# Optimization experiments

Hardware: AMD Instinct MI355X
Metric: run time of the kernel (lower is better)

The kernel has to match this reference:

```python
import jax, jax.numpy as jnp
import numpy as np

N = 100000      # nodes
E = 1200000     # edges
D_IN = 128      # input_dim
H = 64          # hidden_dim
OUT = 3         # output_dim
EPS = 1e-5      # BatchNorm eps


def setup_inputs() -> dict:
    key = jax.random.key(0)
    ks = jax.random.split(key, 24)
    w = lambda k, shape: jax.random.normal(k, shape, jnp.float32) * 0.05
    return {
        "x": jax.random.normal(ks[0], (N, D_IN), jnp.float32),
        "edge_index": jax.random.randint(ks[1], (2, E), 0, N, dtype=jnp.int32),
        "proj_W": w(ks[2], (H, D_IN)), "proj_b": w(ks[3], (H,)),
        "conv1_W": w(ks[4], (H, H)), "conv1_b": w(ks[5], (H,)),
        "bn1_g": jnp.ones((H,), jnp.float32), "bn1_b": w(ks[6], (H,)),
        "conv2_W": w(ks[7], (H, H)), "conv2_b": w(ks[8], (H,)),
        "bn2_g": jnp.ones((H,), jnp.float32), "bn2_b": w(ks[9], (H,)),
        "conv3_W": w(ks[10], (H, H)), "conv3_b": w(ks[11], (H,)),
        "bn3_g": jnp.ones((H,), jnp.float32), "bn3_b": w(ks[12], (H,)),
        "byp_W": w(ks[13], (OUT, D_IN)), "byp_b": w(ks[14], (OUT,)),
        "head_W": w(ks[15], (OUT, H + OUT)), "head_b": w(ks[16], (OUT,)),
    }


def reference(x, edge_index, proj_W, proj_b,
              conv1_W, conv1_b, bn1_g, bn1_b,
              conv2_W, conv2_b, bn2_g, bn2_b,
              conv3_W, conv3_b, bn3_g, bn3_b,
              byp_W, byp_b, head_W, head_b):
    n = x.shape[0]
    row, col = edge_index[0], edge_index[1]
    loop = jnp.arange(n, dtype=row.dtype)
    row_f = jnp.concatenate([row, loop])   # source (with self loops)
    col_f = jnp.concatenate([col, loop])   # target
    # symmetric GCN normalization: deg over targets of A+I, edge weight 1
    deg = jax.ops.segment_sum(jnp.ones(row_f.shape, jnp.float32), col_f, num_segments=n)
    dinv = jnp.where(deg > 0, jax.lax.rsqrt(deg), 0.0)
    norm = dinv[row_f] * dinv[col_f]       # [E+N]

    def gcn(h, W, b):
        h = h @ W.T                                    # transform then propagate
        msg = h[row_f] * norm[:, None]                 # gather + scale
        return jax.ops.segment_sum(msg, col_f, num_segments=n) + b

    def bn(h, g, b):
        # eval-mode BatchNorm1d: running_mean=0, running_var=1 buffers
        return h * (g / jnp.sqrt(1.0 + EPS)) + b

    h = x @ proj_W.T + proj_b
    idn = h
    h = jax.nn.relu(bn(gcn(h, conv1_W, conv1_b), bn1_g, bn1_b)) + idn  # dropout inactive (eval)
    idn = h
    h = jax.nn.relu(bn(gcn(h, conv2_W, conv2_b), bn2_g, bn2_b)) + idn
    h = jax.nn.relu(bn(gcn(h, conv3_W, conv3_b), bn3_g, bn3_b))

    byp = x @ byp_W.T + byp_b
    p = jnp.concatenate([h, byp], axis=1) @ head_W.T + head_b
    kappa = jnp.clip(p[:, 0] * 5.0 + 2.5, 0.2, 10.0)
    alpha = p[:, 1]
    tau = jnp.clip(p[:, 2] + 0.5, 0.05, 2.0)
    return jnp.stack([kappa, alpha, tau], axis=1)
```

## Files before the change

### kernel.cpp

```cpp
#include <hip/hip_runtime.h>
#include <hip/hip_fp16.h>

#define NN 100000
#define NE 1200000
#define NBUK ((NN + 127) / 128)
#define NCHUNK 512

typedef _Float16 h8 __attribute__((ext_vector_type(8)));
typedef float f32x4 __attribute__((ext_vector_type(4)));
typedef float f32x2 __attribute__((ext_vector_type(2)));

__global__ __launch_bounds__(256) void k_bucketA(const int* __restrict__ col,
                                                 int* __restrict__ blkcnt) {
    __shared__ int lh[NBUK];
    const int tid = threadIdx.x;
    const int per = (NE + NCHUNK - 1) / NCHUNK;
    const int e0 = blockIdx.x * per;
    const int e1 = (e0 + per < NE) ? (e0 + per) : NE;
    for (int i = tid; i < NBUK; i += 256) lh[i] = 0;
    __syncthreads();
    for (int e = e0 + tid; e < e1; e += 256)
        atomicAdd(&lh[col[e] >> 7], 1);
    __syncthreads();
    for (int b = tid; b < NBUK; b += 256)
        blkcnt[b * NCHUNK + blockIdx.x] = lh[b];
}

__global__ __launch_bounds__(512) void k_colscan(int* __restrict__ blkcnt, int* __restrict__ bcnt) {
    __shared__ int s[NCHUNK];
    const int b = blockIdx.x, tid = threadIdx.x;
    int v = blkcnt[b * NCHUNK + tid];
    s[tid] = v;
    __syncthreads();
    #pragma unroll
    for (int d = 1; d < NCHUNK; d <<= 1) {
        int t = (tid >= d) ? s[tid - d] : 0;
        __syncthreads();
        s[tid] += t;
        __syncthreads();
    }
    blkcnt[b * NCHUNK + tid] = s[tid] - v;
    if (tid == NCHUNK - 1) bcnt[b] = s[NCHUNK - 1];
}

__global__ __launch_bounds__(1024) void k_bscan(int* __restrict__ bcnt) {
    __shared__ int s[1024];
    int tid = threadIdx.x;
    int v = (tid < NBUK) ? bcnt[tid] : 0;
    s[tid] = v;
    __syncthreads();
    #pragma unroll
    for (int d = 1; d < 1024; d <<= 1) {
        int t = (tid >= d) ? s[tid - d] : 0;
        __syncthreads();
        s[tid] += t;
        __syncthreads();
    }
    if (tid < NBUK) bcnt[tid] = s[tid] - v;
    if (tid == 0) bcnt[NBUK] = NE;
}

__global__ __launch_bounds__(256) void k_bucketB(const int* __restrict__ row,
                                                 const int* __restrict__ col,
                                                 const int* __restrict__ bbase,
                                                 const int* __restrict__ blkcnt,
                                                 unsigned* __restrict__ tmp) {
    __shared__ int lh[NBUK];
    const int tid = threadIdx.x;
    const int per = (NE + NCHUNK - 1) / NCHUNK;
    const int e0 = blockIdx.x * per;
    const int e1 = (e0 + per < NE) ? (e0 + per) : NE;
    for (int b = tid; b < NBUK; b += 256)
        lh[b] = bbase[b] + blkcnt[b * NCHUNK + blockIdx.x];
    __syncthreads();
    for (int e = e0 + tid; e < e1; e += 256) {
        int c = col[e], r = row[e];
        int pos = atomicAdd(&lh[c >> 7], 1);
        tmp[pos] = ((unsigned)r << 7) | (unsigned)(c & 127);
    }
}

__global__ __launch_bounds__(256) void k_build(const unsigned* __restrict__ tmp,
                                               const int* __restrict__ bbase,
                                               int* __restrict__ off,
                                               float* __restrict__ dinv,
                                               int* __restrict__ csr_row) {
    __shared__ int cnt[128], s[128], cur[128];
    const int b = blockIdx.x, tid = threadIdx.x;
    const int colBase = b << 7;
    const int nCols = (NN - colBase < 128) ? (NN - colBase) : 128;
    const int seg0 = bbase[b], seg1 = bbase[b + 1];
    if (tid < 128) cnt[tid] = 0;
    __syncthreads();
    for (int i = seg0 + tid; i < seg1; i += 256)
        atomicAdd(&cnt[tmp[i] & 127], 1);
    __syncthreads();
    if (tid < 128) s[tid] = cnt[tid];
    __syncthreads();
    #pragma unroll
    for (int d = 1; d < 128; d <<= 1) {
        int t = (tid < 128 && tid >= d) ? s[tid - d] : 0;
        __syncthreads();
        if (tid < 128) s[tid] += t;
        __syncthreads();
    }
    if (tid < nCols) {
        int exc = seg0 + s[tid] - cnt[tid];
        off[colBase + tid] = exc;
        cur[tid] = exc;
        dinv[colBase + tid] = rsqrtf((float)cnt[tid] + 1.0f);
    }
    if (b == 0 && tid == 0) off[NN] = NE;
    __syncthreads();
    for (int i = seg0 + tid; i < seg1; i += 256) {
        unsigned v = tmp[i];
        int pos = atomicAdd(&cur[v & 127u], 1);
        csr_row[pos] = (int)(v >> 7);
    }
}

__global__ __launch_bounds__(256) void k_gemmPC(const float* __restrict__ X,
                                                const float* __restrict__ W,
                                                const float* __restrict__ bias,
                                                _Float16* __restrict__ Yh,
                                                const float* __restrict__ bypW,
                                                const float* __restrict__ bypb,
                                                float* __restrict__ bypOut,
                                                const float* __restrict__ convW1,
                                                const float* __restrict__ dinv,
                                                unsigned char* __restrict__ Y8,
                                                int n_nodes) {
    constexpr int D = 128, RS = D + 8, KS = D / 32;
    constexpr int RS2 = 72;
    __shared__ _Float16 Xh[64 * RS];
    __shared__ _Float16 Wh[64 * RS];
    const int tid = threadIdx.x;
    const int n0 = blockIdx.x * 64;

    for (int i = tid; i < 64 * (D / 8); i += 256) {
        int j = i / (D / 8), d8 = (i % (D / 8)) * 8;
        const float4* wp = (const float4*)&W[j * D + d8];
        float4 w0 = wp[0], w1 = wp[1];
        h8 h = { (_Float16)w0.x, (_Float16)w0.y, (_Float16)w0.z, (_Float16)w0.w,
                 (_Float16)w1.x, (_Float16)w1.y, (_Float16)w1.z, (_Float16)w1.w };
        *(h8*)&Wh[j * RS + d8] = h;
    }
    for (int i = tid; i < 64 * (D / 8); i += 256) {
        int nl = i / (D / 8), d8 = (i % (D / 8)) * 8;
        int n = n0 + nl; if (n >= n_nodes) n = n_nodes - 1;
        const float4* xp = (const float4*)&X[(size_t)n * D + d8];
        float4 x0 = xp[0], x1 = xp[1];
        h8 h = { (_Float16)x0.x, (_Float16)x0.y, (_Float16)x0.z, (_Float16)x0.w,
                 (_Float16)x1.x, (_Float16)x1.y, (_Float16)x1.z, (_Float16)x1.w };
        *(h8*)&Xh[nl * RS + d8] = h;
    }
    __syncthreads();

    const int wid = tid >> 6, lane = tid & 63;
    const int lm = lane & 15, lq = lane >> 4;
    const int mBase = wid * 16;

    h8 bfrag[4][KS];
    #pragma unroll
    for (int t = 0; t < 4; ++t)
        #pragma unroll
        for (int s = 0; s < KS; ++s)
            bfrag[t][s] = *(const h8*)&Wh[(t * 16 + lm) * RS + s * 32 + lq * 8];

    h8 bfragB[KS];
    #pragma unroll
    for (int s = 0; s < KS; ++s) {
        if (lm < 3) {
            const float4* wp = (const float4*)&bypW[lm * D + s * 32 + lq * 8];
            float4 w0 = wp[0], w1 = wp[1];
            bfragB[s] = (h8){ (_Float16)w0.x, (_Float16)w0.y, (_Float16)w0.z, (_Float16)w0.w,
                              (_Float16)w1.x, (_Float16)w1.y, (_Float16)w1.z, (_Float16)w1.w };
        } else {
            bfragB[s] = (h8)(_Float16)0;
        }
    }

    f32x4 acc[5] = {};
    #pragma unroll
    for (int s = 0; s < KS; ++s) {
        h8 a = *(const h8*)&Xh[(mBase + lm) * RS + s * 32 + lq * 8];
        #pragma unroll
        for (int t = 0; t < 4; ++t)
            acc[t] = __builtin_amdgcn_mfma_f32_16x16x32_f16(a, bfrag[t][s], acc[t], 0, 0, 0);
        acc[4] = __builtin_amdgcn_mfma_f32_16x16x32_f16(a, bfragB[s], acc[4], 0, 0, 0);
    }

    float bb[4];
    #pragma unroll
    for (int t = 0; t < 4; ++t) bb[t] = bias[t * 16 + lm];
    float bypbv = (lm < 3) ? bypb[lm] : 0.f;
    const int nodeBase = n0 + mBase + lq * 4;

    __syncthreads();

    #pragma unroll
    for (int r = 0; r < 4; ++r) {
        int node = nodeBase + r;
        int nloc = mBase + lq * 4 + r;
        #pragma unroll
        for (int t = 0; t < 4; ++t) {
            _Float16 hv = (_Float16)(acc[t][r] + bb[t]);
            Xh[nloc * RS2 + t * 16 + lm] = hv;
            if (node < n_nodes)
                Yh[(size_t)node * 64 + t * 16 + lm] = hv;
        }
        if (node < n_nodes && lm < 3)
            bypOut[node * 3 + lm] = acc[4][r] + bypbv;
    }
    for (int i = tid; i < 64 * 8; i += 256) {
        int j = i >> 3, d8 = (i & 7) * 8;
        const float4* wp = (const float4*)&convW1[j * 64 + d8];
        float4 w0 = wp[0], w1 = wp[1];
        h8 h = { (_Float16)w0.x, (_Float16)w0.y, (_Float16)w0.z, (_Float16)w0.w,
                 (_Float16)w1.x, (_Float16)w1.y, (_Float16)w1.z, (_Float16)w1.w };
        *(h8*)&Wh[j * RS2 + d8] = h;
    }
    __syncthreads();

    h8 cfrag[4][2];
    #pragma unroll
    for (int t = 0; t < 4; ++t)
        #pragma unroll
        for (int s = 0; s < 2; ++s)
            cfrag[t][s] = *(const h8*)&Wh[(t * 16 + lm) * RS2 + s * 32 + lq * 8];

    f32x4 acc2[4] = {};
    #pragma unroll
    for (int s = 0; s < 2; ++s) {
        h8 a = *(const h8*)&Xh[(mBase + lm) * RS2 + s * 32 + lq * 8];
        #pragma unroll
        for (int t = 0; t < 4; ++t)
            acc2[t] = __builtin_amdgcn_mfma_f32_16x16x32_f16(a, cfrag[t][s], acc2[t], 0, 0, 0);
    }
    #pragma unroll
    for (int r = 0; r < 4; ++r) {
        int node = nodeBase + r;
        if (node < n_nodes) {
            float sdv = dinv[node];
            #pragma unroll
            for (int t = 0; t < 4; ++t) {
                float v = acc2[t][r] * sdv;
                int pk = __builtin_amdgcn_cvt_pk_fp8_f32(v, v, 0, false);
                Y8[(size_t)node * 64 + t * 16 + lm] = (unsigned char)(pk & 0xff);
            }
        }
    }
}

__global__ __launch_bounds__(256) void k_gemmC(const _Float16* __restrict__ Xhg,
                                               const float* __restrict__ W,
                                               const float* __restrict__ dinv,
                                               unsigned char* __restrict__ Y8,
                                               int n_nodes) {
    constexpr int D = 64, RS = D + 8, KS = D / 32;
    __shared__ _Float16 Xh[64 * RS];
    __shared__ _Float16 Wh[64 * RS];
    const int tid = threadIdx.x;
    const int n0 = blockIdx.x * 64;

    for (int i = tid; i < 64 * (D / 8); i += 256) {
        int j = i / (D / 8), d8 = (i % (D / 8)) * 8;
        const float4* wp = (const float4*)&W[j * D + d8];
        float4 w0 = wp[0], w1 = wp[1];
        h8 h = { (_Float16)w0.x, (_Float16)w0.y, (_Float16)w0.z, (_Float16)w0.w,
                 (_Float16)w1.x, (_Float16)w1.y, (_Float16)w1.z, (_Float16)w1.w };
        *(h8*)&Wh[j * RS + d8] = h;
    }
    for (int i = tid; i < 64 * (D / 8); i += 256) {
        int nl = i / (D / 8), d8 = (i % (D / 8)) * 8;
        int n = n0 + nl; if (n >= n_nodes) n = n_nodes - 1;
        *(h8*)&Xh[nl * RS + d8] = *(const h8*)&Xhg[(size_t)n * D + d8];
    }
    __syncthreads();

    const int wid = tid >> 6, lane = tid & 63;
    const int lm = lane & 15, lq = lane >> 4;
    const int mBase = wid * 16;

    h8 bfrag[4][KS];
    #pragma unroll
    for (int t = 0; t < 4; ++t)
        #pragma unroll
        for (int s = 0; s < KS; ++s)
            bfrag[t][s] = *(const h8*)&Wh[(t * 16 + lm) * RS + s * 32 + lq * 8];

    f32x4 acc[4] = {};
    #pragma unroll
    for (int s = 0; s < KS; ++s) {
        h8 a = *(const h8*)&Xh[(mBase + lm) * RS + s * 32 + lq * 8];
        #pragma unroll
        for (int t = 0; t < 4; ++t)
            acc[t] = __builtin_amdgcn_mfma_f32_16x16x32_f16(a, bfrag[t][s], acc[t], 0, 0, 0);
    }

    const int nodeBase = n0 + mBase + lq * 4;
    #pragma unroll
    for (int r = 0; r < 4; ++r) {
        int node = nodeBase + r;
        if (node < n_nodes) {
            float sdv = dinv[node];
            #pragma unroll
            for (int t = 0; t < 4; ++t) {
                float v = acc[t][r] * sdv;
                int pk = __builtin_amdgcn_cvt_pk_fp8_f32(v, v, 0, false);
                Y8[(size_t)node * 64 + t * 16 + lm] = (unsigned char)(pk & 0xff);
            }
        }
    }
}

template<bool RES, bool HEAD>
__global__ __launch_bounds__(256) void k_gather(const unsigned char* __restrict__ hB8,
                                                const float* __restrict__ dinv,
                                                const int* __restrict__ off,
                                                const int* __restrict__ csr_row,
                                                const float* __restrict__ convb,
                                                const float* __restrict__ bng,
                                                const float* __restrict__ bnb,
                                                _Float16* __restrict__ hA,
                                                const float* __restrict__ byp,
                                                const float* __restrict__ headW,
                                                const float* __restrict__ headb,
                                                float* __restrict__ out) {
    __shared__ float HWs[HEAD ? 204 : 1];
    const int tid = threadIdx.x;
    if constexpr (HEAD) {
        for (int i = tid; i < 204; i += 256)
            HWs[i] = (i < 201) ? headW[i] : headb[i - 201];
        __syncthreads();
    }
    const int wid = tid >> 6, lane = tid & 63;
    const int n = blockIdx.x * 32 + wid * 8 + (lane >> 3);
    const int oct = lane & 7;
    const int f0 = oct * 8;

    const int e0 = off[n], eEnd = off[n + 1];
    const int deg = eEnd - e0;
    int m = deg;
    #pragma unroll
    for (int mask = 8; mask < 64; mask <<= 1) {
        int o = __shfl_xor(m, mask, 64);
        m = (o > m) ? o : m;
    }

    const uint2* rows8 = (const uint2*)hB8;
    float acc[8] = {0, 0, 0, 0, 0, 0, 0, 0};
    uint2 selfw = rows8[(size_t)n * 8 + oct];
    {
        f32x2 p0 = __builtin_amdgcn_cvt_pk_f32_fp8(selfw.x, false);
        f32x2 p1 = __builtin_amdgcn_cvt_pk_f32_fp8(selfw.x, true);
        f32x2 p2 = __builtin_amdgcn_cvt_pk_f32_fp8(selfw.y, false);
        f32x2 p3 = __builtin_amdgcn_cvt_pk_f32_fp8(selfw.y, true);
        acc[0] += p0.x; acc[1] += p0.y; acc[2] += p1.x; acc[3] += p1.y;
        acc[4] += p2.x; acc[5] += p2.y; acc[6] += p3.x; acc[7] += p3.y;
    }
    for (int it = 0; it < m; it += 8) {
        uint2 w[8];
        #pragma unroll
        for (int q = 0; q < 8; ++q) {
            bool vq = it + q < deg;
            int rq = csr_row[vq ? e0 + it + q : 0];
            w[q] = rows8[(size_t)rq * 8 + oct];
            if (!vq) { w[q].x = 0; w[q].y = 0; }
        }
        #pragma unroll
        for (int q = 0; q < 8; ++q) {
            f32x2 p0 = __builtin_amdgcn_cvt_pk_f32_fp8(w[q].x, false);
            f32x2 p1 = __builtin_amdgcn_cvt_pk_f32_fp8(w[q].x, true);
            f32x2 p2 = __builtin_amdgcn_cvt_pk_f32_fp8(w[q].y, false);
            f32x2 p3 = __builtin_amdgcn_cvt_pk_f32_fp8(w[q].y, true);
            acc[0] += p0.x; acc[1] += p0.y; acc[2] += p1.x; acc[3] += p1.y;
            acc[4] += p2.x; acc[5] += p2.y; acc[6] += p3.x; acc[7] += p3.y;
        }
    }

    const float dv = dinv[n];
    const float bnscale = rsqrtf(1.0f + 1e-5f);
    const float4 cb0 = *(const float4*)&convb[f0], cb1 = *(const float4*)&convb[f0 + 4];
    const float4 g0  = *(const float4*)&bng[f0],  g1  = *(const float4*)&bng[f0 + 4];
    const float4 b0_ = *(const float4*)&bnb[f0],  b1_ = *(const float4*)&bnb[f0 + 4];
    const float cb[8] = { cb0.x, cb0.y, cb0.z, cb0.w, cb1.x, cb1.y, cb1.z, cb1.w };
    const float gg[8] = { g0.x, g0.y, g0.z, g0.w, g1.x, g1.y, g1.z, g1.w };
    const float bb[8] = { b0_.x, b0_.y, b0_.z, b0_.w, b1_.x, b1_.y, b1_.z, b1_.w };
    float v[8];
    #pragma unroll
    for (int j = 0; j < 8; ++j)
        v[j] = fmaxf((acc[j] * dv + cb[j]) * (gg[j] * bnscale) + bb[j], 0.0f);

    if constexpr (!HEAD) {
        size_t o = ((size_t)n << 6) + f0;
        if constexpr (RES) {
            h8 old = *(const h8*)&hA[o];
            #pragma unroll
            for (int j = 0; j < 8; ++j) v[j] += (float)old[j];
        }
        h8 res = { (_Float16)v[0], (_Float16)v[1], (_Float16)v[2], (_Float16)v[3],
                   (_Float16)v[4], (_Float16)v[5], (_Float16)v[6], (_Float16)v[7] };
        *(h8*)&hA[o] = res;
    } else {
        float p[3];
        #pragma unroll
        for (int o = 0; o < 3; ++o) {
            float t = 0.f;
            #pragma unroll
            for (int j = 0; j < 8; ++j) t += v[j] * HWs[o * 67 + f0 + j];
            p[o] = t;
        }
        #pragma unroll
        for (int mask = 1; mask < 8; mask <<= 1) {
            #pragma unroll
            for (int o = 0; o < 3; ++o) p[o] += __shfl_xor(p[o], mask, 64);
        }
        if (oct == 0) {
            float by0 = byp[n * 3], by1 = byp[n * 3 + 1], by2 = byp[n * 3 + 2];
            #pragma unroll
            for (int o = 0; o < 3; ++o)
                p[o] += by0 * HWs[o * 67 + 64] + by1 * HWs[o * 67 + 65] + by2 * HWs[o * 67 + 66]
                      + HWs[201 + o];
            float kappa = fminf(fmaxf(p[0] * 5.0f + 2.5f, 0.2f), 10.0f);
            float tau   = fminf(fmaxf(p[2] + 0.5f, 0.05f), 2.0f);
            out[(size_t)n * 3]     = kappa;
            out[(size_t)n * 3 + 1] = p[1];
            out[(size_t)n * 3 + 2] = tau;
        }
    }
}

extern "C" void kernel_launch(void* const* d_in, const int* in_sizes, int n_in,
                              void* d_out, int out_size, void* d_ws, size_t ws_size,
                              hipStream_t stream) {
    const float* x     = (const float*)d_in[0];
    const int*   ei    = (const int*)d_in[1];
    const int*   row   = ei;
    const int*   col   = ei + NE;
    const float* projW = (const float*)d_in[2];
    const float* projb = (const float*)d_in[3];
    const float* convW[3] = { (const float*)d_in[4], (const float*)d_in[8],  (const float*)d_in[12] };
    const float* convb[3] = { (const float*)d_in[5], (const float*)d_in[9],  (const float*)d_in[13] };
    const float* bng[3]   = { (const float*)d_in[6], (const float*)d_in[10], (const float*)d_in[14] };
    const float* bnb[3]   = { (const float*)d_in[7], (const float*)d_in[11], (const float*)d_in[15] };
    const float* bypW  = (const float*)d_in[16];
    const float* bypb  = (const float*)d_in[17];
    const float* headW = (const float*)d_in[18];
    const float* headb = (const float*)d_in[19];
    float* out = (float*)d_out;

    float*    ws   = (float*)d_ws;
    float*    dinv = ws;
    _Float16* hAh  = (_Float16*)(ws + 102400);
    unsigned char* hB8 = (unsigned char*)(hAh + (size_t)NN * 64);
    float*    byp  = (float*)(hB8 + (size_t)NN * 64);
    int*      off     = (int*)(byp + 300032);
    int*      csr_row = off + 100096;
    int*      bcnt    = csr_row + NE;
    int*      blkcnt  = bcnt + 784;
    unsigned* tmp     = (unsigned*)hAh;

    k_bucketA<<<NCHUNK, 256, 0, stream>>>(col, blkcnt);
    k_colscan<<<NBUK, NCHUNK, 0, stream>>>(blkcnt, bcnt);
    k_bscan<<<1, 1024, 0, stream>>>(bcnt);
    k_bucketB<<<NCHUNK, 256, 0, stream>>>(row, col, bcnt, blkcnt, tmp);
    k_build<<<NBUK, 256, 0, stream>>>(tmp, bcnt, off, dinv, csr_row);

    k_gemmPC<<<(NN + 63) / 64, 256, 0, stream>>>(
        x, projW, projb, hAh, bypW, bypb, byp, convW[0], dinv, hB8, NN);

    for (int l = 0; l < 3; l++) {
        if (l > 0)
            k_gemmC<<<(NN + 63) / 64, 256, 0, stream>>>(hAh, convW[l], dinv, hB8, NN);
        if (l < 2)
            k_gather<true, false><<<NN / 32, 256, 0, stream>>>(
                hB8, dinv, off, csr_row, convb[l], bng[l], bnb[l], hAh,
                nullptr, nullptr, nullptr, nullptr);
        else
            k_gather<false, true><<<NN / 32, 256, 0, stream>>>(
                hB8, dinv, off, csr_row, convb[l], bng[l], bnb[l], nullptr,
                byp, headW, headb, out);
    }
}
```

Baseline: 256.8 us.

## Fuse next-layer GEMM into gather epilogue and merge scan kernels

The separate per-layer transform GEMM kernel is removed and its work moved into the gather kernel's epilogue. Each block stages its 32 freshly aggregated fp16 rows in shared memory and multiplies them by the next layer's weights with MFMA, writing fp8 output into a ping-pong buffer. The bucket-count scans are merged into one launch, with bucket totals accumulated atomically after a memset, and the gather loop now iterates per node degree rather than the max degree across the wave. This removes two kernel launches and one round trip of the hidden state through memory per layer. In exchange the gather kernel uses more shared memory and a block barrier, and needs an extra fp8 buffer.

```diff
diff --git a/kernel.cpp b/kernel.cpp
--- a/kernel.cpp
+++ b/kernel.cpp
@@ -11,7 +11,8 @@
 typedef float f32x2 __attribute__((ext_vector_type(2)));
 
 __global__ __launch_bounds__(256) void k_bucketA(const int* __restrict__ col,
-                                                 int* __restrict__ blkcnt) {
+                                                 int* __restrict__ blkcnt,
+                                                 int* __restrict__ bcnt) {
     __shared__ int lh[NBUK];
     const int tid = threadIdx.x;
     const int per = (NE + NCHUNK - 1) / NCHUNK;
@@ -22,42 +23,43 @@
     for (int e = e0 + tid; e < e1; e += 256)
         atomicAdd(&lh[col[e] >> 7], 1);
     __syncthreads();
-    for (int b = tid; b < NBUK; b += 256)
-        blkcnt[b * NCHUNK + blockIdx.x] = lh[b];
-}
-
-__global__ __launch_bounds__(512) void k_colscan(int* __restrict__ blkcnt, int* __restrict__ bcnt) {
-    __shared__ int s[NCHUNK];
+    for (int b = tid; b < NBUK; b += 256) {
+        int v = lh[b];
+        blkcnt[b * NCHUNK + blockIdx.x] = v;
+        if (v) atomicAdd(&bcnt[b], v);
+    }
+}
+
+__global__ __launch_bounds__(1024) void k_scanAll(int* __restrict__ blkcnt,
+                                                  int* __restrict__ bcnt) {
+    __shared__ int s[1024];
     const int b = blockIdx.x, tid = threadIdx.x;
-    int v = blkcnt[b * NCHUNK + tid];
-    s[tid] = v;
-    __syncthreads();
-    #pragma unroll
-    for (int d = 1; d < NCHUNK; d <<= 1) {
-        int t = (tid >= d) ? s[tid - d] : 0;
-        __syncthreads();
-        s[tid] += t;
-        __syncthreads();
-    }
-    blkcnt[b * NCHUNK + tid] = s[tid] - v;
-    if (tid == NCHUNK - 1) bcnt[b] = s[NCHUNK - 1];
-}
-
-__global__ __launch_bounds__(1024) void k_bscan(int* __restrict__ bcnt) {
-    __shared__ int s[1024];
-    int tid = threadIdx.x;
-    int v = (tid < NBUK) ? bcnt[tid] : 0;
-    s[tid] = v;
-    __syncthreads();
-    #pragma unroll
-    for (int d = 1; d < 1024; d <<= 1) {
-        int t = (tid >= d) ? s[tid - d] : 0;
-        __syncthreads();
-        s[tid] += t;
-        __syncthreads();
-    }
-    if (tid < NBUK) bcnt[tid] = s[tid] - v;
-    if (tid == 0) bcnt[NBUK] = NE;
+    if (b < NBUK) {
+        int v = (tid < NCHUNK) ? blkcnt[b * NCHUNK + tid] : 0;
+        s[tid] = v;
+        __syncthreads();
+        #pragma unroll
+        for (int d = 1; d < 1024; d <<= 1) {
+            int t = (tid >= d) ? s[tid - d] : 0;
+            __syncthreads();
+            s[tid] += t;
+            __syncthreads();
+        }
+        if (tid < NCHUNK) blkcnt[b * NCHUNK + tid] = s[tid] - v;
+    } else {
+        int v = (tid < NBUK) ? bcnt[tid] : 0;
+        s[tid] = v;
+        __syncthreads();
+        #pragma unroll
+        for (int d = 1; d < 1024; d <<= 1) {
+            int t = (tid >= d) ? s[tid - d] : 0;
+            __syncthreads();
+            s[tid] += t;
+            __syncthreads();
+        }
+        if (tid < NBUK) bcnt[tid] = s[tid] - v;
+        if (tid == 0) bcnt[NBUK] = NE;
+    }
 }
 
 __global__ __launch_bounds__(256) void k_bucketB(const int* __restrict__ row,
@@ -252,69 +254,16 @@
     }
 }
 
-__global__ __launch_bounds__(256) void k_gemmC(const _Float16* __restrict__ Xhg,
-                                               const float* __restrict__ W,
-                                               const float* __restrict__ dinv,
-                                               unsigned char* __restrict__ Y8,
-                                               int n_nodes) {
-    constexpr int D = 64, RS = D + 8, KS = D / 32;
-    __shared__ _Float16 Xh[64 * RS];
-    __shared__ _Float16 Wh[64 * RS];
-    const int tid = threadIdx.x;
-    const int n0 = blockIdx.x * 64;
-
-    for (int i = tid; i < 64 * (D / 8); i += 256) {
-        int j = i / (D / 8), d8 = (i % (D / 8)) * 8;
-        const float4* wp = (const float4*)&W[j * D + d8];
-        float4 w0 = wp[0], w1 = wp[1];
-        h8 h = { (_Float16)w0.x, (_Float16)w0.y, (_Float16)w0.z, (_Float16)w0.w,
-                 (_Float16)w1.x, (_Float16)w1.y, (_Float16)w1.z, (_Float16)w1.w };
-        *(h8*)&Wh[j * RS + d8] = h;
-    }
-    for (int i = tid; i < 64 * (D / 8); i += 256) {
-        int nl = i / (D / 8), d8 = (i % (D / 8)) * 8;
-        int n = n0 + nl; if (n >= n_nodes) n = n_nodes - 1;
-        *(h8*)&Xh[nl * RS + d8] = *(const h8*)&Xhg[(size_t)n * D + d8];
-    }
-    __syncthreads();
-
-    const int wid = tid >> 6, lane = tid & 63;
-    const int lm = lane & 15, lq = lane >> 4;
-    const int mBase = wid * 16;
-
-    h8 bfrag[4][KS];
-    #pragma unroll
-    for (int t = 0; t < 4; ++t)
-        #pragma unroll
-        for (int s = 0; s < KS; ++s)
-            bfrag[t][s] = *(const h8*)&Wh[(t * 16 + lm) * RS + s * 32 + lq * 8];
-
-    f32x4 acc[4] = {};
-    #pragma unroll
-    for (int s = 0; s < KS; ++s) {
-        h8 a = *(const h8*)&Xh[(mBase + lm) * RS + s * 32 + lq * 8];
-        #pragma unroll
-        for (int t = 0; t < 4; ++t)
-            acc[t] = __builtin_amdgcn_mfma_f32_16x16x32_f16(a, bfrag[t][s], acc[t], 0, 0, 0);
-    }
-
-    const int nodeBase = n0 + mBase + lq * 4;
-    #pragma unroll
-    for (int r = 0; r < 4; ++r) {
-        int node = nodeBase + r;
-        if (node < n_nodes) {
-            float sdv = dinv[node];
-            #pragma unroll
-            for (int t = 0; t < 4; ++t) {
-                float v = acc[t][r] * sdv;
-                int pk = __builtin_amdgcn_cvt_pk_fp8_f32(v, v, 0, false);
-                Y8[(size_t)node * 64 + t * 16 + lm] = (unsigned char)(pk & 0xff);
-            }
-        }
-    }
-}
-
-template<bool RES, bool HEAD>
+__device__ __forceinline__ void acc_fp8(float* acc, uint2 w) {
+    f32x2 p0 = __builtin_amdgcn_cvt_pk_f32_fp8(w.x, false);
+    f32x2 p1 = __builtin_amdgcn_cvt_pk_f32_fp8(w.x, true);
+    f32x2 p2 = __builtin_amdgcn_cvt_pk_f32_fp8(w.y, false);
+    f32x2 p3 = __builtin_amdgcn_cvt_pk_f32_fp8(w.y, true);
+    acc[0] += p0.x; acc[1] += p0.y; acc[2] += p1.x; acc[3] += p1.y;
+    acc[4] += p2.x; acc[5] += p2.y; acc[6] += p3.x; acc[7] += p3.y;
+}
+
+template<bool HEAD>
 __global__ __launch_bounds__(256) void k_gather(const unsigned char* __restrict__ hB8,
                                                 const float* __restrict__ dinv,
                                                 const int* __restrict__ off,
@@ -323,60 +272,56 @@
                                                 const float* __restrict__ bng,
                                                 const float* __restrict__ bnb,
                                                 _Float16* __restrict__ hA,
+                                                const float* __restrict__ nextW,
+                                                unsigned char* __restrict__ Y8,
                                                 const float* __restrict__ byp,
                                                 const float* __restrict__ headW,
                                                 const float* __restrict__ headb,
                                                 float* __restrict__ out) {
+    constexpr int RS2 = 72;
+    __shared__ _Float16 Ws[HEAD ? 1 : 64 * RS2];
+    __shared__ _Float16 Hs[HEAD ? 1 : 32 * RS2];
     __shared__ float HWs[HEAD ? 204 : 1];
     const int tid = threadIdx.x;
     if constexpr (HEAD) {
         for (int i = tid; i < 204; i += 256)
             HWs[i] = (i < 201) ? headW[i] : headb[i - 201];
         __syncthreads();
+    } else {
+        for (int i = tid; i < 64 * 8; i += 256) {
+            int j = i >> 3, d8 = (i & 7) * 8;
+            const float4* wp = (const float4*)&nextW[j * 64 + d8];
+            float4 w0 = wp[0], w1 = wp[1];
+            h8 h = { (_Float16)w0.x, (_Float16)w0.y, (_Float16)w0.z, (_Float16)w0.w,
+                     (_Float16)w1.x, (_Float16)w1.y, (_Float16)w1.z, (_Float16)w1.w };
+            *(h8*)&Ws[j * RS2 + d8] = h;
+        }
     }
     const int wid = tid >> 6, lane = tid & 63;
-    const int n = blockIdx.x * 32 + wid * 8 + (lane >> 3);
+    const int nloc = wid * 8 + (lane >> 3);
+    const int n = blockIdx.x * 32 + nloc;
     const int oct = lane & 7;
     const int f0 = oct * 8;
 
-    const int e0 = off[n], eEnd = off[n + 1];
-    const int deg = eEnd - e0;
-    int m = deg;
-    #pragma unroll
-    for (int mask = 8; mask < 64; mask <<= 1) {
-        int o = __shfl_xor(m, mask, 64);
-        m = (o > m) ? o : m;
-    }
+    const int e0 = off[n];
+    const int deg = off[n + 1] - e0;
 
     const uint2* rows8 = (const uint2*)hB8;
     float acc[8] = {0, 0, 0, 0, 0, 0, 0, 0};
-    uint2 selfw = rows8[(size_t)n * 8 + oct];
-    {
-        f32x2 p0 = __builtin_amdgcn_cvt_pk_f32_fp8(selfw.x, false);
-        f32x2 p1 = __builtin_amdgcn_cvt_pk_f32_fp8(selfw.x, true);
-        f32x2 p2 = __builtin_amdgcn_cvt_pk_f32_fp8(selfw.y, false);
-        f32x2 p3 = __builtin_amdgcn_cvt_pk_f32_fp8(selfw.y, true);
-        acc[0] += p0.x; acc[1] += p0.y; acc[2] += p1.x; acc[3] += p1.y;
-        acc[4] += p2.x; acc[5] += p2.y; acc[6] += p3.x; acc[7] += p3.y;
-    }
-    for (int it = 0; it < m; it += 8) {
+    acc_fp8(acc, rows8[(size_t)n * 8 + oct]);
+
+    for (int it = 0; it < deg; it += 8) {
+        const int rem = deg - it;
         uint2 w[8];
         #pragma unroll
         for (int q = 0; q < 8; ++q) {
-            bool vq = it + q < deg;
-            int rq = csr_row[vq ? e0 + it + q : 0];
+            int rq = csr_row[e0 + it + ((q < rem) ? q : 0)];
             w[q] = rows8[(size_t)rq * 8 + oct];
-            if (!vq) { w[q].x = 0; w[q].y = 0; }
-        }
-        #pragma unroll
-        for (int q = 0; q < 8; ++q) {
-            f32x2 p0 = __builtin_amdgcn_cvt_pk_f32_fp8(w[q].x, false);
-            f32x2 p1 = __builtin_amdgcn_cvt_pk_f32_fp8(w[q].x, true);
-            f32x2 p2 = __builtin_amdgcn_cvt_pk_f32_fp8(w[q].y, false);
-            f32x2 p3 = __builtin_amdgcn_cvt_pk_f32_fp8(w[q].y, true);
-            acc[0] += p0.x; acc[1] += p0.y; acc[2] += p1.x; acc[3] += p1.y;
-            acc[4] += p2.x; acc[5] += p2.y; acc[6] += p3.x; acc[7] += p3.y;
-        }
+            if (q >= rem) { w[q].x = 0; w[q].y = 0; }
+        }
+        #pragma unroll
+        for (int q = 0; q < 8; ++q)
+            acc_fp8(acc, w[q]);
     }
 
     const float dv = dinv[n];
@@ -394,14 +339,45 @@
 
     if constexpr (!HEAD) {
         size_t o = ((size_t)n << 6) + f0;
-        if constexpr (RES) {
-            h8 old = *(const h8*)&hA[o];
-            #pragma unroll
-            for (int j = 0; j < 8; ++j) v[j] += (float)old[j];
-        }
+        h8 old = *(const h8*)&hA[o];
+        #pragma unroll
+        for (int j = 0; j < 8; ++j) v[j] += (float)old[j];
         h8 res = { (_Float16)v[0], (_Float16)v[1], (_Float16)v[2], (_Float16)v[3],
                    (_Float16)v[4], (_Float16)v[5], (_Float16)v[6], (_Float16)v[7] };
         *(h8*)&hA[o] = res;
+        *(h8*)&Hs[nloc * RS2 + f0] = res;
+        __syncthreads();
+
+        const int lm = lane & 15, lq = lane >> 4;
+        const int mt = (wid & 1) * 16;
+        const int nt = (wid >> 1) * 32;
+        h8 afrag[2], bfrag[2][2];
+        #pragma unroll
+        for (int s = 0; s < 2; ++s)
+            afrag[s] = *(const h8*)&Hs[(mt + lm) * RS2 + s * 32 + lq * 8];
+        #pragma unroll
+        for (int t = 0; t < 2; ++t)
+            #pragma unroll
+            for (int s = 0; s < 2; ++s)
+                bfrag[t][s] = *(const h8*)&Ws[(nt + t * 16 + lm) * RS2 + s * 32 + lq * 8];
+        f32x4 acc2[2] = {};
+        #pragma unroll
+        for (int s = 0; s < 2; ++s)
+            #pragma unroll
+            for (int t = 0; t < 2; ++t)
+                acc2[t] = __builtin_amdgcn_mfma_f32_16x16x32_f16(afrag[s], bfrag[t][s], acc2[t], 0, 0, 0);
+        const int nodeBase = blockIdx.x * 32 + mt + lq * 4;
+        #pragma unroll
+        for (int r = 0; r < 4; ++r) {
+            int node = nodeBase + r;
+            float sdv = dinv[node];
+            #pragma unroll
+            for (int t = 0; t < 2; ++t) {
+                float vv = acc2[t][r] * sdv;
+                int pk = __builtin_amdgcn_cvt_pk_fp8_f32(vv, vv, 0, false);
+                Y8[(size_t)node * 64 + nt + t * 16 + lm] = (unsigned char)(pk & 0xff);
+            }
+        }
     } else {
         float p[3];
         #pragma unroll
@@ -453,33 +429,31 @@
     float*    ws   = (float*)d_ws;
     float*    dinv = ws;
     _Float16* hAh  = (_Float16*)(ws + 102400);
-    unsigned char* hB8 = (unsigned char*)(hAh + (size_t)NN * 64);
-    float*    byp  = (float*)(hB8 + (size_t)NN * 64);
+    unsigned char* hB8a = (unsigned char*)(hAh + (size_t)NN * 64);
+    float*    byp  = (float*)(hB8a + (size_t)NN * 64);
     int*      off     = (int*)(byp + 300032);
     int*      csr_row = off + 100096;
     int*      bcnt    = csr_row + NE;
     int*      blkcnt  = bcnt + 784;
+    unsigned char* hB8b = (unsigned char*)(blkcnt + (size_t)NBUK * NCHUNK);
     unsigned* tmp     = (unsigned*)hAh;
 
-    k_bucketA<<<NCHUNK, 256, 0, stream>>>(col, blkcnt);
-    k_colscan<<<NBUK, NCHUNK, 0, stream>>>(blkcnt, bcnt);
-    k_bscan<<<1, 1024, 0, stream>>>(bcnt);
+    hipMemsetAsync(bcnt, 0, 784 * sizeof(int), stream);
+    k_bucketA<<<NCHUNK, 256, 0, stream>>>(col, blkcnt, bcnt);
+    k_scanAll<<<NBUK + 1, 1024, 0, stream>>>(blkcnt, bcnt);
     k_bucketB<<<NCHUNK, 256, 0, stream>>>(row, col, bcnt, blkcnt, tmp);
     k_build<<<NBUK, 256, 0, stream>>>(tmp, bcnt, off, dinv, csr_row);
 
     k_gemmPC<<<(NN + 63) / 64, 256, 0, stream>>>(
-        x, projW, projb, hAh, bypW, bypb, byp, convW[0], dinv, hB8, NN);
-
-    for (int l = 0; l < 3; l++) {
-        if (l > 0)
-            k_gemmC<<<(NN + 63) / 64, 256, 0, stream>>>(hAh, convW[l], dinv, hB8, NN);
-        if (l < 2)
-            k_gather<true, false><<<NN / 32, 256, 0, stream>>>(
-                hB8, dinv, off, csr_row, convb[l], bng[l], bnb[l], hAh,
-                nullptr, nullptr, nullptr, nullptr);
-        else
-            k_gather<false, true><<<NN / 32, 256, 0, stream>>>(
-                hB8, dinv, off, csr_row, convb[l], bng[l], bnb[l], nullptr,
-                byp, headW, headb, out);
-    }
-}
+        x, projW, projb, hAh, bypW, bypb, byp, convW[0], dinv, hB8a, NN);
+
+    k_gather<false><<<NN / 32, 256, 0, stream>>>(
+        hB8a, dinv, off, csr_row, convb[0], bng[0], bnb[0], hAh,
+        convW[1], hB8b, nullptr, nullptr, nullptr, nullptr);
+    k_gather<false><<<NN / 32, 256, 0, stream>>>(
+        hB8b, dinv, off, csr_row, convb[1], bng[1], bnb[1], hAh,
+        convW[2], hB8a, nullptr, nullptr, nullptr, nullptr);
+    k_gather<true><<<NN / 32, 256, 0, stream>>>(
+        hB8a, dinv, off, csr_row, convb[2], bng[2], bnb[2], nullptr,
+        nullptr, nullptr, byp, headW, headb, out);
+}
```

Measured after the change: 258.2 us. About the same (+0.5%).
